# Optimization experiments

Measured on AMD Instinct MI355X. Metric: run time of the kernel, lower is better.

## Reference

```python
import jax, jax.numpy as jnp
import numpy as np

B, C, O, H, W, K, KS = 32, 128, 128, 56, 56, 4, 3
EPS = 1e-5


def setup_inputs() -> dict:
    key = jax.random.key(0)
    ks = jax.random.split(key, 6)
    sc = lambda k, shape, s: jax.random.normal(k, shape, jnp.float32) * s
    return {
        "x": jax.random.normal(ks[0], (B, C, H, W), jnp.float32),
        "fc1_w": sc(ks[1], (K, C), 0.05),
        "fc1_b": jnp.zeros((K,), jnp.float32),
        "fc2_w": sc(ks[2], (K, K), 0.3),
        "fc2_b": jnp.zeros((K,), jnp.float32),
        "weight": sc(ks[3], (K, O, C, KS, KS), 0.05),  # [K, out, in/groups, kh, kw]
        "bias": sc(ks[4], (K, O), 0.05),
        "gamma": jnp.ones((O,), jnp.float32),
        "beta": jnp.zeros((O,), jnp.float32),
    }


def reference(x, fc1_w, fc1_b, fc2_w, fc2_b, weight, bias, gamma, beta):
    # attention2d: global avg pool -> 1x1 conv (== linear) -> relu -> 1x1 conv -> softmax over K
    pooled = x.mean(axis=(2, 3))                          # [B, C]
    h = jax.nn.relu(pooled @ fc1_w.T + fc1_b)             # [B, K]
    attn = jax.nn.softmax(h @ fc2_w.T + fc2_b, axis=-1)   # [B, K]

    # per-sample aggregated kernel / bias
    agg_w = jnp.einsum('bk,koihw->boihw', attn, weight)   # [B, O, C, KS, KS]
    agg_b = attn @ bias                                    # [B, O]

    # per-sample conv (== groups=batch trick in torch)
    def conv_one(xi, wi):
        return jax.lax.conv_general_dilated(
            xi[None], wi, window_strides=(1, 1),
            padding=((1, 1), (1, 1)),
            dimension_numbers=('NCHW', 'OIHW', 'NCHW'))[0]

    out = jax.vmap(conv_one)(x, agg_w) + agg_b[:, :, None, None]  # [B, O, H, W]

    # BatchNorm2d in training mode: biased batch stats over (N, H, W)
    mean = out.mean(axis=(0, 2, 3))
    var = out.var(axis=(0, 2, 3))
    out = (out - mean[None, :, None, None]) * jax.lax.rsqrt(var + EPS)[None, :, None, None]
    out = out * gamma[None, :, None, None] + beta[None, :, None, None]
    return jax.nn.relu(out)
```

## Files before the change

kernel.cpp:

```cpp
#include <hip/hip_runtime.h>
#include <hip/hip_bf16.h>

#define BB 32
#define CC 128
#define OO 128
#define HH 56
#define WW 56
#define KK 4
#define HW 3136
#define WPLANE 147456
#define EPSV 1e-5f

#define NPOS 348
#define BUFB 22528

typedef __attribute__((ext_vector_type(8))) short short8v;
typedef __attribute__((ext_vector_type(4))) float f32x4;

static __device__ __forceinline__ void gload16(const void* g, void* l) {
    __builtin_amdgcn_global_load_lds((const __attribute__((address_space(1))) void*)g,
                                     (__attribute__((address_space(3))) void*)l, 16, 0, 0);
}

__global__ void convert_pool_kernel(const float* __restrict__ x,
                                    ushort* __restrict__ xbf,
                                    float* __restrict__ pooledp,
                                    ushort* __restrict__ zpage) {
    const int h = blockIdx.x, b = blockIdx.y;
    if (h == 0 && b == 0 && threadIdx.x < 32) zpage[threadIdx.x] = 0;
    __shared__ float xl[128 * 57];
    const float* xp = x + (size_t)(b * CC) * HW + h * WW;
    #pragma unroll
    for (int k = 0; k < 28; ++k) {
        int e = threadIdx.x + k * 256;
        int c = e / 56, w = e - c * 56;
        xl[c * 57 + w] = xp[(size_t)c * HW + w];
    }
    __syncthreads();
    ushort* op = xbf + ((size_t)(b * HH + h)) * WW * CC;
    #pragma unroll
    for (int k = 0; k < 7; ++k) {
        int f = threadIdx.x + k * 256;
        int w = f >> 5, c4 = (f & 31) * 4;
        ushort4 v;
        __hip_bfloat16 b0 = __float2bfloat16(xl[(c4 + 0) * 57 + w]);
        __hip_bfloat16 b1 = __float2bfloat16(xl[(c4 + 1) * 57 + w]);
        __hip_bfloat16 b2 = __float2bfloat16(xl[(c4 + 2) * 57 + w]);
        __hip_bfloat16 b3 = __float2bfloat16(xl[(c4 + 3) * 57 + w]);
        v.x = *(ushort*)&b0; v.y = *(ushort*)&b1;
        v.z = *(ushort*)&b2; v.w = *(ushort*)&b3;
        *(ushort4*)(op + (size_t)w * CC + c4) = v;
    }
    if (threadIdx.x < 128) {
        int c = threadIdx.x;
        float s = 0.f;
        #pragma unroll
        for (int w = 0; w < 56; ++w) s += xl[c * 57 + w];
        pooledp[((size_t)(b * HH + h)) * CC + c] = s;
    }
}

__global__ void attn_kernel(const float* __restrict__ pooledp,
                            const float* __restrict__ fc1_w, const float* __restrict__ fc1_b,
                            const float* __restrict__ fc2_w, const float* __restrict__ fc2_b,
                            float* __restrict__ attn) {
    const int b = blockIdx.x, c = threadIdx.x;
    float s = 0.f;
    for (int h = 0; h < HH; ++h) s += pooledp[((size_t)(b * HH + h)) * CC + c];
    const float pc = s * (1.0f / HW);
    __shared__ float red[8];
    const int lane = c & 63, wid = c >> 6;
    #pragma unroll
    for (int k = 0; k < KK; ++k) {
        float v = pc * fc1_w[k * CC + c];
        for (int off = 32; off > 0; off >>= 1) v += __shfl_down(v, off, 64);
        if (lane == 0) red[k * 2 + wid] = v;
    }
    __syncthreads();
    if (c == 0) {
        float hk[KK], z[KK], m = -1e30f, den = 0.f;
        #pragma unroll
        for (int k = 0; k < KK; ++k)
            hk[k] = fmaxf(red[k * 2] + red[k * 2 + 1] + fc1_b[k], 0.f);
        #pragma unroll
        for (int k = 0; k < KK; ++k) {
            float t = fc2_b[k];
            #pragma unroll
            for (int j = 0; j < KK; ++j) t += hk[j] * fc2_w[k * KK + j];
            z[k] = t; m = fmaxf(m, t);
        }
        #pragma unroll
        for (int k = 0; k < KK; ++k) { z[k] = expf(z[k] - m); den += z[k]; }
        #pragma unroll
        for (int k = 0; k < KK; ++k) attn[b * KK + k] = z[k] / den;
    }
}

__global__ void aggw_kernel(const float* __restrict__ attn, const float* __restrict__ weight,
                            const float* __restrict__ bias,
                            ushort* __restrict__ aggw, float* __restrict__ agg_b) {
    int idx = blockIdx.x * 256 + threadIdx.x;
    if (idx < BB * 9 * OO * CC) {
        int cc = idx & 31;
        int t1 = idx >> 5;
        int o  = t1 & 127;
        int t2 = t1 >> 7;
        int ci = t2 & 3;
        int t3 = t2 >> 2;
        int j  = t3 % 9;
        int b  = t3 / 9;
        int c  = ci * 32 + cc;
        size_t wi = ((size_t)(o * CC + c)) * 9 + j;
        float s = attn[b*KK + 0] * weight[wi]
                + attn[b*KK + 1] * weight[wi + (size_t)WPLANE]
                + attn[b*KK + 2] * weight[wi + (size_t)2*WPLANE]
                + attn[b*KK + 3] * weight[wi + (size_t)3*WPLANE];
        __hip_bfloat16 hb = __float2bfloat16(s);
        aggw[idx] = *(ushort*)&hb;
    }
    if (blockIdx.x < 16) {
        int i = blockIdx.x * 256 + threadIdx.x;
        int b = i >> 7, o = i & 127;
        float s = 0.f;
        #pragma unroll
        for (int k = 0; k < KK; ++k) s += attn[b*KK + k] * bias[k*OO + o];
        agg_b[i] = s;
    }
}

__launch_bounds__(256, 2)
__global__ void conv_kernel(const ushort* __restrict__ xbf, const ushort* __restrict__ aggw,
                            const float* __restrict__ agg_b, const ushort* __restrict__ zpage,
                            float* __restrict__ out,
                            float* __restrict__ psum, float* __restrict__ psumsq) {
    const int lid  = blockIdx.x;
    const int gwid = (lid & 7) * 56 + (lid >> 3);
    const int b = gwid / 14;
    const int t = gwid - b * 14;
    const int h0 = t * 4;
    __shared__ ushort xs[2 * BUFB / 2];

    const int tid  = threadIdx.x;
    const int lane = tid & 63;
    const int wid  = tid >> 6;
    const int wg = wid & 1;
    const int wy = wid >> 1;
    const int cf = lane & 15;
    const int kg = lane >> 4;

    const ushort* gp[6]; int gstep[6];
    #pragma unroll
    for (int k = 0; k < 6; ++k) {
        int q = wid + 4 * k;
        int un = q * 64 + lane;
        int u = un ^ ((un >> 3) & 7);
        int pos = u >> 2, quad = u & 3;
        int row = pos / 58, col = pos - row * 58;
        int gh = h0 - 1 + row, gw = col - 1;
        bool valid = (pos < NPOS) && (gh >= 0) && (gh < HH) && (gw >= 0) && (gw < WW);
        gp[k] = valid ? (xbf + ((size_t)((b * HH + gh) * WW + gw)) * CC + quad * 8) : zpage;
        gstep[k] = valid ? 32 : 0;
    }

    int blin[7];
    #pragma unroll
    for (int nf = 0; nf < 7; ++nf) {
        int p = wy * 112 + nf * 16 + cf;
        int r = p / 56, w = p - r * 56;
        blin[nf] = (((r + 1) * 58 + (w + 1)) << 6) + kg * 16;
    }

    f32x4 acc[4][7];
    #pragma unroll
    for (int mf = 0; mf < 4; ++mf)
        #pragma unroll
        for (int nf = 0; nf < 7; ++nf) acc[mf][nf] = (f32x4){0.f, 0.f, 0.f, 0.f};

    const ushort* Ab = aggw + ((size_t)b * 36) * 4096 + (size_t)(wg * 64 + cf) * 32 + kg * 8;
    #define ALOAD(mf_, j_, ci_) (*(const short8v*)(Ab + (size_t)((j_) * 4 + (ci_)) * 4096 + (mf_) * 512))

    short8v pa[4];
    #pragma unroll
    for (int mf = 0; mf < 4; ++mf) pa[mf] = ALOAD(mf, 0, 0);

    #pragma unroll
    for (int k = 0; k < 6; ++k) {
        int q = wid + 4 * k;
        if (q < 22) { gload16(gp[k], (char*)xs + q * 1024); gp[k] += gstep[k]; }
    }
    __syncthreads();

    int cur = 0;
    for (int ci = 0; ci < 4; ++ci) {
        if (ci < 3) {
            char* base = (char*)xs + (cur ^ 1) * BUFB;
            #pragma unroll
            for (int k = 0; k < 6; ++k) {
                int q = wid + 4 * k;
                if (q < 22) { gload16(gp[k], base + q * 1024); gp[k] += gstep[k]; }
            }
        }
        const char* xbuf = (const char*)xs + cur * BUFB;

        short8v bfc[7], bfn[7];
        #pragma unroll
        for (int nf = 0; nf < 7; ++nf) {
            int lin = blin[nf] + (-58 - 1) * 64;
            int swz = lin ^ ((lin >> 3) & 0x70);
            bfc[nf] = *(const short8v*)(xbuf + swz);
        }
        #pragma unroll
        for (int j = 0; j < 9; ++j) {
            if (j < 8) {
                const int toff = (((j+1)/3 - 1) * 58 + ((j+1)%3 - 1)) * 64;
                #pragma unroll
                for (int nf = 0; nf < 7; ++nf) {
                    int lin = blin[nf] + toff;
                    int swz = lin ^ ((lin >> 3) & 0x70);
                    bfn[nf] = *(const short8v*)(xbuf + swz);
                }
            }
            short8v ca[4];
            #pragma unroll
            for (int mf = 0; mf < 4; ++mf) ca[mf] = pa[mf];
            if (j < 8) {
                #pragma unroll
                for (int mf = 0; mf < 4; ++mf) pa[mf] = ALOAD(mf, j + 1, ci);
            } else if (ci < 3) {
                #pragma unroll
                for (int mf = 0; mf < 4; ++mf) pa[mf] = ALOAD(mf, 0, ci + 1);
            }
            #pragma unroll
            for (int nf = 0; nf < 7; ++nf) {
                #pragma unroll
                for (int mf = 0; mf < 4; ++mf)
                    acc[mf][nf] = __builtin_amdgcn_mfma_f32_16x16x32_bf16(ca[mf], bfc[nf], acc[mf][nf], 0, 0, 0);
            }
            if (j < 8) {
                #pragma unroll
                for (int nf = 0; nf < 7; ++nf) bfc[nf] = bfn[nf];
            }
        }
        if (ci < 3) __syncthreads();
        cur ^= 1;
    }

    #pragma unroll
    for (int mf = 0; mf < 4; ++mf) {
        #pragma unroll
        for (int i = 0; i < 4; ++i) {
            const int o = wg * 64 + mf * 16 + kg * 4 + i;
            const float ab = agg_b[b * OO + o];
            float* op = out + ((size_t)(b * OO + o)) * HW;
            float s = 0.f, s2 = 0.f;
            #pragma unroll
            for (int nf = 0; nf < 7; ++nf) {
                int p = wy * 112 + nf * 16 + cf;
                int r = p / 56, w = p - r * 56;
                float v = acc[mf][nf][i] + ab;
                op[(h0 + r) * WW + w] = v;
                s += v; s2 += v * v;
            }
            s  += __shfl_xor(s, 1, 64);  s  += __shfl_xor(s, 2, 64);
            s  += __shfl_xor(s, 4, 64);  s  += __shfl_xor(s, 8, 64);
            s2 += __shfl_xor(s2, 1, 64); s2 += __shfl_xor(s2, 2, 64);
            s2 += __shfl_xor(s2, 4, 64); s2 += __shfl_xor(s2, 8, 64);
            if (cf == 0) {
                int row = (b * 14 + t) * 2 + wy;
                psum[row * OO + o]   = s;
                psumsq[row * OO + o] = s2;
            }
        }
    }
}

__global__ void finstats_kernel(const float* __restrict__ psum, const float* __restrict__ psumsq,
                                float* __restrict__ sums, float* __restrict__ sumsq) {
    const int o = blockIdx.x, l = threadIdx.x;
    float s = 0.f, s2 = 0.f;
    for (int r = l; r < 896; r += 64) { s += psum[r * OO + o]; s2 += psumsq[r * OO + o]; }
    for (int off = 32; off > 0; off >>= 1) {
        s  += __shfl_down(s, off, 64);
        s2 += __shfl_down(s2, off, 64);
    }
    if (l == 0) { sums[o] = s; sumsq[o] = s2; }
}

__global__ void bn_kernel(float* __restrict__ out,
                          const float* __restrict__ sums, const float* __restrict__ sumsq,
                          const float* __restrict__ gamma, const float* __restrict__ beta) {
    const float invN = 1.0f / (float)(BB * HW);
    const int total4 = BB * OO * HW / 4;
    for (int i = blockIdx.x * blockDim.x + threadIdx.x; i < total4; i += gridDim.x * blockDim.x) {
        int o = (i / (HW/4)) % OO;
        float mean = sums[o] * invN;
        float var  = sumsq[o] * invN - mean*mean;
        float inv  = rsqrtf(var + EPSV);
        float g  = gamma[o] * inv;
        float bt = beta[o] - mean * g;
        float4 v = ((float4*)out)[i];
        v.x = fmaxf(v.x*g + bt, 0.f);
        v.y = fmaxf(v.y*g + bt, 0.f);
        v.z = fmaxf(v.z*g + bt, 0.f);
        v.w = fmaxf(v.w*g + bt, 0.f);
        ((float4*)out)[i] = v;
    }
}

extern "C" void kernel_launch(void* const* d_in, const int* in_sizes, int n_in,
                              void* d_out, int out_size, void* d_ws, size_t ws_size,
                              hipStream_t stream) {
    const float* x      = (const float*)d_in[0];
    const float* fc1_w  = (const float*)d_in[1];
    const float* fc1_b  = (const float*)d_in[2];
    const float* fc2_w  = (const float*)d_in[3];
    const float* fc2_b  = (const float*)d_in[4];
    const float* weight = (const float*)d_in[5];
    const float* bias   = (const float*)d_in[6];
    const float* gamma  = (const float*)d_in[7];
    const float* beta   = (const float*)d_in[8];
    float* out = (float*)d_out;

    const size_t XBF_ELEMS  = (size_t)BB * HW * CC;
    const size_t AGGW_ELEMS = (size_t)BB * 9 * OO * CC;
    ushort* xbf  = (ushort*)d_ws;
    ushort* aggw = xbf + XBF_ELEMS;
    float*  wsf  = (float*)(aggw + AGGW_ELEMS);
    float* pooledp = wsf;
    float* attn    = pooledp + 229376;
    float* agg_b   = attn + 128;
    float* psum    = agg_b + 4096;
    float* psumsq  = psum + 114688;
    float* sums    = psumsq + 114688;
    float* sumsq   = sums + 128;
    ushort* zpage  = (ushort*)(sumsq + 128);

    convert_pool_kernel<<<dim3(HH, BB), 256, 0, stream>>>(x, xbf, pooledp, zpage);
    attn_kernel<<<BB, 128, 0, stream>>>(pooledp, fc1_w, fc1_b, fc2_w, fc2_b, attn);
    aggw_kernel<<<(int)((AGGW_ELEMS + 255)/256), 256, 0, stream>>>(attn, weight, bias, aggw, agg_b);
    conv_kernel<<<dim3(448), 256, 0, stream>>>(xbf, aggw, agg_b, zpage, out, psum, psumsq);
    finstats_kernel<<<OO, 64, 0, stream>>>(psum, psumsq, sums, sumsq);
    bn_kernel<<<2048, 256, 0, stream>>>(out, sums, sumsq, gamma, beta);
}
```

Measured before the change: 111.2 us.

## Fuse conv, batch-stat reduction and BN/ReLU into one cooperative kernel

Replaces the conv, finstats and bn launches with a single cooperative-launch kernel. It keeps conv accumulators in registers, reduces per-channel stats across the grid with two grid syncs, then writes normalized ReLU output directly. This removes the round trip of writing and rereading the full fp32 output. To fit co-residency it switches the fused path to a single LDS buffer without double-buffered prefetch, and it falls back to the old three kernels if the cooperative launch fails. The convert/pool kernel also now uses float4 loads into a swizzled LDS layout and writes 16-byte bf16 vectors.

```diff
diff --git a/kernel.cpp b/kernel.cpp
--- a/kernel.cpp
+++ b/kernel.cpp
@@ -1,5 +1,8 @@
 #include <hip/hip_runtime.h>
 #include <hip/hip_bf16.h>
+#include <hip/hip_cooperative_groups.h>
+
+namespace cg = cooperative_groups;
 
 #define BB 32
 #define CC 128
@@ -28,34 +31,45 @@
                                     ushort* __restrict__ zpage) {
     const int h = blockIdx.x, b = blockIdx.y;
     if (h == 0 && b == 0 && threadIdx.x < 32) zpage[threadIdx.x] = 0;
-    __shared__ float xl[128 * 57];
+    __shared__ float4 xl4[1792];
     const float* xp = x + (size_t)(b * CC) * HW + h * WW;
-    #pragma unroll
-    for (int k = 0; k < 28; ++k) {
-        int e = threadIdx.x + k * 256;
-        int c = e / 56, w = e - c * 56;
-        xl[c * 57 + w] = xp[(size_t)c * HW + w];
+
+    #pragma unroll
+    for (int k = 0; k < 7; ++k) {
+        int u = threadIdx.x + k * 256;
+        int c = u / 14, w4 = u - c * 14;
+        float4 v = *(const float4*)(xp + (size_t)c * HW + w4 * 4);
+        xl4[u ^ ((c >> 3) & 7)] = v;
     }
     __syncthreads();
-    ushort* op = xbf + ((size_t)(b * HH + h)) * WW * CC;
-    #pragma unroll
-    for (int k = 0; k < 7; ++k) {
-        int f = threadIdx.x + k * 256;
-        int w = f >> 5, c4 = (f & 31) * 4;
-        ushort4 v;
-        __hip_bfloat16 b0 = __float2bfloat16(xl[(c4 + 0) * 57 + w]);
-        __hip_bfloat16 b1 = __float2bfloat16(xl[(c4 + 1) * 57 + w]);
-        __hip_bfloat16 b2 = __float2bfloat16(xl[(c4 + 2) * 57 + w]);
-        __hip_bfloat16 b3 = __float2bfloat16(xl[(c4 + 3) * 57 + w]);
-        v.x = *(ushort*)&b0; v.y = *(ushort*)&b1;
-        v.z = *(ushort*)&b2; v.w = *(ushort*)&b3;
-        *(ushort4*)(op + (size_t)w * CC + c4) = v;
-    }
+
+    const float* xf = (const float*)xl4;
+    #pragma unroll
+    for (int k = 0; k < 4; ++k) {
+        int v = threadIdx.x + k * 256;
+        if (v < 896) {
+            int w = v >> 4, c8 = v & 15;
+            int w4 = w >> 2, wo = w & 3;
+            short8v res;
+            #pragma unroll
+            for (int j = 0; j < 8; ++j) {
+                int c = c8 * 8 + j;
+                int su = (c * 14 + w4) ^ (c8 & 7);
+                __hip_bfloat16 hb = __float2bfloat16(xf[su * 4 + wo]);
+                res[j] = *(short*)&hb;
+            }
+            *(short8v*)(xbf + ((size_t)((b * HH + h) * WW + w)) * CC + c8 * 8) = res;
+        }
+    }
+
     if (threadIdx.x < 128) {
         int c = threadIdx.x;
         float s = 0.f;
         #pragma unroll
-        for (int w = 0; w < 56; ++w) s += xl[c * 57 + w];
+        for (int w4 = 0; w4 < 14; ++w4) {
+            float4 v = xl4[(c * 14 + w4) ^ ((c >> 3) & 7)];
+            s += v.x + v.y + v.z + v.w;
+        }
         pooledp[((size_t)(b * HH + h)) * CC + c] = s;
     }
 }
@@ -128,6 +142,115 @@
     }
 }
 
+template <bool DBUF>
+static __device__ __forceinline__ void conv_body(
+        const ushort* __restrict__ xbf, const ushort* __restrict__ aggw,
+        const ushort* __restrict__ zpage, ushort* xs,
+        int b, int h0, int wg, int wy, int cf, int kg, int wid, int lane,
+        f32x4 (&acc)[4][7]) {
+    const ushort* gp[6]; int gstep[6];
+    #pragma unroll
+    for (int k = 0; k < 6; ++k) {
+        int q = wid + 4 * k;
+        int un = q * 64 + lane;
+        int u = un ^ ((un >> 3) & 7);
+        int pos = u >> 2, quad = u & 3;
+        int row = pos / 58, col = pos - row * 58;
+        int gh = h0 - 1 + row, gw = col - 1;
+        bool valid = (pos < NPOS) && (gh >= 0) && (gh < HH) && (gw >= 0) && (gw < WW);
+        gp[k] = valid ? (xbf + ((size_t)((b * HH + gh) * WW + gw)) * CC + quad * 8) : zpage;
+        gstep[k] = valid ? 32 : 0;
+    }
+
+    int blin[7];
+    #pragma unroll
+    for (int nf = 0; nf < 7; ++nf) {
+        int p = wy * 112 + nf * 16 + cf;
+        int r = p / 56, w = p - r * 56;
+        blin[nf] = (((r + 1) * 58 + (w + 1)) << 6) + kg * 16;
+    }
+
+    const ushort* Ab = aggw + ((size_t)b * 36) * 4096 + (size_t)(wg * 64 + cf) * 32 + kg * 8;
+    #define ALOAD(mf_, j_, ci_) (*(const short8v*)(Ab + (size_t)((j_) * 4 + (ci_)) * 4096 + (mf_) * 512))
+
+    short8v pa[4];
+    #pragma unroll
+    for (int mf = 0; mf < 4; ++mf) pa[mf] = ALOAD(mf, 0, 0);
+
+    #pragma unroll
+    for (int k = 0; k < 6; ++k) {
+        int q = wid + 4 * k;
+        if (q < 22) { gload16(gp[k], (char*)xs + q * 1024); gp[k] += gstep[k]; }
+    }
+    __syncthreads();
+
+    int cur = 0;
+    for (int ci = 0; ci < 4; ++ci) {
+        if (DBUF && ci < 3) {
+            char* base = (char*)xs + (cur ^ 1) * BUFB;
+            #pragma unroll
+            for (int k = 0; k < 6; ++k) {
+                int q = wid + 4 * k;
+                if (q < 22) { gload16(gp[k], base + q * 1024); gp[k] += gstep[k]; }
+            }
+        }
+        const char* xbuf = (const char*)xs + (DBUF ? cur * BUFB : 0);
+
+        short8v bfc[7], bfn[7];
+        #pragma unroll
+        for (int nf = 0; nf < 7; ++nf) {
+            int lin = blin[nf] + (-58 - 1) * 64;
+            int swz = lin ^ ((lin >> 3) & 0x70);
+            bfc[nf] = *(const short8v*)(xbuf + swz);
+        }
+        #pragma unroll
+        for (int j = 0; j < 9; ++j) {
+            if (j < 8) {
+                const int toff = (((j+1)/3 - 1) * 58 + ((j+1)%3 - 1)) * 64;
+                #pragma unroll
+                for (int nf = 0; nf < 7; ++nf) {
+                    int lin = blin[nf] + toff;
+                    int swz = lin ^ ((lin >> 3) & 0x70);
+                    bfn[nf] = *(const short8v*)(xbuf + swz);
+                }
+            }
+            short8v ca[4];
+            #pragma unroll
+            for (int mf = 0; mf < 4; ++mf) ca[mf] = pa[mf];
+            if (j < 8) {
+                #pragma unroll
+                for (int mf = 0; mf < 4; ++mf) pa[mf] = ALOAD(mf, j + 1, ci);
+            } else if (ci < 3) {
+                #pragma unroll
+                for (int mf = 0; mf < 4; ++mf) pa[mf] = ALOAD(mf, 0, ci + 1);
+            }
+            #pragma unroll
+            for (int nf = 0; nf < 7; ++nf) {
+                #pragma unroll
+                for (int mf = 0; mf < 4; ++mf)
+                    acc[mf][nf] = __builtin_amdgcn_mfma_f32_16x16x32_bf16(ca[mf], bfc[nf], acc[mf][nf], 0, 0, 0);
+            }
+            if (j < 8) {
+                #pragma unroll
+                for (int nf = 0; nf < 7; ++nf) bfc[nf] = bfn[nf];
+            }
+        }
+        if (ci < 3) {
+            if (!DBUF) {
+                __syncthreads();
+                #pragma unroll
+                for (int k = 0; k < 6; ++k) {
+                    int q = wid + 4 * k;
+                    if (q < 22) { gload16(gp[k], (char*)xs + q * 1024); gp[k] += gstep[k]; }
+                }
+            }
+            __syncthreads();
+            cur ^= 1;
+        }
+    }
+    #undef ALOAD
+}
+
 __launch_bounds__(256, 2)
 __global__ void conv_kernel(const ushort* __restrict__ xbf, const ushort* __restrict__ aggw,
                             const float* __restrict__ agg_b, const ushort* __restrict__ zpage,
@@ -143,32 +266,8 @@
     const int tid  = threadIdx.x;
     const int lane = tid & 63;
     const int wid  = tid >> 6;
-    const int wg = wid & 1;
-    const int wy = wid >> 1;
-    const int cf = lane & 15;
-    const int kg = lane >> 4;
-
-    const ushort* gp[6]; int gstep[6];
-    #pragma unroll
-    for (int k = 0; k < 6; ++k) {
-        int q = wid + 4 * k;
-        int un = q * 64 + lane;
-        int u = un ^ ((un >> 3) & 7);
-        int pos = u >> 2, quad = u & 3;
-        int row = pos / 58, col = pos - row * 58;
-        int gh = h0 - 1 + row, gw = col - 1;
-        bool valid = (pos < NPOS) && (gh >= 0) && (gh < HH) && (gw >= 0) && (gw < WW);
-        gp[k] = valid ? (xbf + ((size_t)((b * HH + gh) * WW + gw)) * CC + quad * 8) : zpage;
-        gstep[k] = valid ? 32 : 0;
-    }
-
-    int blin[7];
-    #pragma unroll
-    for (int nf = 0; nf < 7; ++nf) {
-        int p = wy * 112 + nf * 16 + cf;
-        int r = p / 56, w = p - r * 56;
-        blin[nf] = (((r + 1) * 58 + (w + 1)) << 6) + kg * 16;
-    }
+    const int wg = wid & 1, wy = wid >> 1;
+    const int cf = lane & 15, kg = lane >> 4;
 
     f32x4 acc[4][7];
     #pragma unroll
@@ -176,74 +275,7 @@
         #pragma unroll
         for (int nf = 0; nf < 7; ++nf) acc[mf][nf] = (f32x4){0.f, 0.f, 0.f, 0.f};
 
-    const ushort* Ab = aggw + ((size_t)b * 36) * 4096 + (size_t)(wg * 64 + cf) * 32 + kg * 8;
-    #define ALOAD(mf_, j_, ci_) (*(const short8v*)(Ab + (size_t)((j_) * 4 + (ci_)) * 4096 + (mf_) * 512))
-
-    short8v pa[4];
-    #pragma unroll
-    for (int mf = 0; mf < 4; ++mf) pa[mf] = ALOAD(mf, 0, 0);
-
-    #pragma unroll
-    for (int k = 0; k < 6; ++k) {
-        int q = wid + 4 * k;
-        if (q < 22) { gload16(gp[k], (char*)xs + q * 1024); gp[k] += gstep[k]; }
-    }
-    __syncthreads();
-
-    int cur = 0;
-    for (int ci = 0; ci < 4; ++ci) {
-        if (ci < 3) {
-            char* base = (char*)xs + (cur ^ 1) * BUFB;
-            #pragma unroll
-            for (int k = 0; k < 6; ++k) {
-                int q = wid + 4 * k;
-                if (q < 22) { gload16(gp[k], base + q * 1024); gp[k] += gstep[k]; }
-            }
-        }
-        const char* xbuf = (const char*)xs + cur * BUFB;
-
-        short8v bfc[7], bfn[7];
-        #pragma unroll
-        for (int nf = 0; nf < 7; ++nf) {
-            int lin = blin[nf] + (-58 - 1) * 64;
-            int swz = lin ^ ((lin >> 3) & 0x70);
-            bfc[nf] = *(const short8v*)(xbuf + swz);
-        }
-        #pragma unroll
-        for (int j = 0; j < 9; ++j) {
-            if (j < 8) {
-                const int toff = (((j+1)/3 - 1) * 58 + ((j+1)%3 - 1)) * 64;
-                #pragma unroll
-                for (int nf = 0; nf < 7; ++nf) {
-                    int lin = blin[nf] + toff;
-                    int swz = lin ^ ((lin >> 3) & 0x70);
-                    bfn[nf] = *(const short8v*)(xbuf + swz);
-                }
-            }
-            short8v ca[4];
-            #pragma unroll
-            for (int mf = 0; mf < 4; ++mf) ca[mf] = pa[mf];
-            if (j < 8) {
-                #pragma unroll
-                for (int mf = 0; mf < 4; ++mf) pa[mf] = ALOAD(mf, j + 1, ci);
-            } else if (ci < 3) {
-                #pragma unroll
-                for (int mf = 0; mf < 4; ++mf) pa[mf] = ALOAD(mf, 0, ci + 1);
-            }
-            #pragma unroll
-            for (int nf = 0; nf < 7; ++nf) {
-                #pragma unroll
-                for (int mf = 0; mf < 4; ++mf)
-                    acc[mf][nf] = __builtin_amdgcn_mfma_f32_16x16x32_bf16(ca[mf], bfc[nf], acc[mf][nf], 0, 0, 0);
-            }
-            if (j < 8) {
-                #pragma unroll
-                for (int nf = 0; nf < 7; ++nf) bfc[nf] = bfn[nf];
-            }
-        }
-        if (ci < 3) __syncthreads();
-        cur ^= 1;
-    }
+    conv_body<true>(xbf, aggw, zpage, xs, b, h0, wg, wy, cf, kg, wid, lane, acc);
 
     #pragma unroll
     for (int mf = 0; mf < 4; ++mf) {
@@ -269,6 +301,109 @@
                 int row = (b * 14 + t) * 2 + wy;
                 psum[row * OO + o]   = s;
                 psumsq[row * OO + o] = s2;
+            }
+        }
+    }
+}
+
+__launch_bounds__(256, 2)
+__global__ void conv_bn_kernel(const ushort* __restrict__ xbf, const ushort* __restrict__ aggw,
+                               const float* __restrict__ agg_b, const ushort* __restrict__ zpage,
+                               float* __restrict__ out,
+                               float* __restrict__ psum, float* __restrict__ psumsq,
+                               float* __restrict__ sums, float* __restrict__ sumsq,
+                               const float* __restrict__ gamma, const float* __restrict__ beta) {
+    const int lid  = blockIdx.x;
+    const int gwid = (lid & 7) * 56 + (lid >> 3);
+    const int b = gwid / 14;
+    const int t = gwid - b * 14;
+    const int h0 = t * 4;
+    __shared__ ushort xs[BUFB / 2];
+
+    const int tid  = threadIdx.x;
+    const int lane = tid & 63;
+    const int wid  = tid >> 6;
+    const int wg = wid & 1, wy = wid >> 1;
+    const int cf = lane & 15, kg = lane >> 4;
+
+    f32x4 acc[4][7];
+    #pragma unroll
+    for (int mf = 0; mf < 4; ++mf)
+        #pragma unroll
+        for (int nf = 0; nf < 7; ++nf) acc[mf][nf] = (f32x4){0.f, 0.f, 0.f, 0.f};
+
+    conv_body<false>(xbf, aggw, zpage, xs, b, h0, wg, wy, cf, kg, wid, lane, acc);
+
+    #pragma unroll
+    for (int mf = 0; mf < 4; ++mf) {
+        #pragma unroll
+        for (int i = 0; i < 4; ++i) {
+            const int o = wg * 64 + mf * 16 + kg * 4 + i;
+            const float ab = agg_b[b * OO + o];
+            float s = 0.f, s2 = 0.f;
+            #pragma unroll
+            for (int nf = 0; nf < 7; ++nf) {
+                float v = acc[mf][nf][i] + ab;
+                acc[mf][nf][i] = v;
+                s += v; s2 += v * v;
+            }
+            s  += __shfl_xor(s, 1, 64);  s  += __shfl_xor(s, 2, 64);
+            s  += __shfl_xor(s, 4, 64);  s  += __shfl_xor(s, 8, 64);
+            s2 += __shfl_xor(s2, 1, 64); s2 += __shfl_xor(s2, 2, 64);
+            s2 += __shfl_xor(s2, 4, 64); s2 += __shfl_xor(s2, 8, 64);
+            if (cf == 0) {
+                int row = (b * 14 + t) * 2 + wy;
+                psum[row * OO + o]   = s;
+                psumsq[row * OO + o] = s2;
+            }
+        }
+    }
+
+    cg::grid_group grid = cg::this_grid();
+    grid.sync();
+
+    if (lid < 128) {
+        const int o = lid;
+        float s = 0.f, s2 = 0.f;
+        for (int r = tid; r < 896; r += 256) {
+            s  += psum[r * OO + o];
+            s2 += psumsq[r * OO + o];
+        }
+        for (int off = 32; off > 0; off >>= 1) {
+            s  += __shfl_down(s, off, 64);
+            s2 += __shfl_down(s2, off, 64);
+        }
+        float* red = (float*)xs;
+        if (lane == 0) { red[wid] = s; red[8 + wid] = s2; }
+        __syncthreads();
+        if (tid == 0) {
+            sums[o]  = red[0] + red[1] + red[2] + red[3];
+            sumsq[o] = red[8] + red[9] + red[10] + red[11];
+        }
+    }
+    grid.sync();
+
+    float* sl = (float*)xs;
+    if (tid < 128) { sl[tid] = sums[tid]; sl[128 + tid] = sumsq[tid]; }
+    __syncthreads();
+
+    const float invN = 1.0f / (float)(BB * HW);
+    #pragma unroll
+    for (int mf = 0; mf < 4; ++mf) {
+        #pragma unroll
+        for (int i = 0; i < 4; ++i) {
+            const int o = wg * 64 + mf * 16 + kg * 4 + i;
+            float mean = sl[o] * invN;
+            float var  = sl[128 + o] * invN - mean * mean;
+            float inv  = rsqrtf(var + EPSV);
+            float g  = gamma[o] * inv;
+            float bt = beta[o] - mean * g;
+            float* op = out + ((size_t)(b * OO + o)) * HW;
+            #pragma unroll
+            for (int nf = 0; nf < 7; ++nf) {
+                int p = wy * 112 + nf * 16 + cf;
+                int r = p / 56, w = p - r * 56;
+                op[(h0 + r) * WW + w] = fmaxf(acc[mf][nf][i] * g + bt, 0.f);
             }
         }
     }
@@ -338,7 +473,16 @@
     convert_pool_kernel<<<dim3(HH, BB), 256, 0, stream>>>(x, xbf, pooledp, zpage);
     attn_kernel<<<BB, 128, 0, stream>>>(pooledp, fc1_w, fc1_b, fc2_w, fc2_b, attn);
     aggw_kernel<<<(int)((AGGW_ELEMS + 255)/256), 256, 0, stream>>>(attn, weight, bias, aggw, agg_b);
-    conv_kernel<<<dim3(448), 256, 0, stream>>>(xbf, aggw, agg_b, zpage, out, psum, psumsq);
-    finstats_kernel<<<OO, 64, 0, stream>>>(psum, psumsq, sums, sumsq);
-    bn_kernel<<<2048, 256, 0, stream>>>(out, sums, sumsq, gamma, beta);
-}
+
+    void* cargs[] = { (void*)&xbf, (void*)&aggw, (void*)&agg_b, (void*)&zpage,
+                      (void*)&out, (void*)&psum, (void*)&psumsq,
+                      (void*)&sums, (void*)&sumsq, (void*)&gamma, (void*)&beta };
+    hipError_t cerr = hipLaunchCooperativeKernel((const void*)conv_bn_kernel,
+                                                 dim3(448), dim3(256), cargs, 0, stream);
+    if (cerr != hipSuccess) {
+        (void)hipGetLastError();
+        conv_kernel<<<dim3(448), 256, 0, stream>>>(xbf, aggw, agg_b, zpage, out, psum, psumsq);
+        finstats_kernel<<<OO, 64, 0, stream>>>(psum, psumsq, sums, sumsq);
+        bn_kernel<<<2048, 256, 0, stream>>>(out, sums, sumsq, gamma, beta);
+    }
+}
```

Measured after the change: 247.5 us. 2.22x slower.

## Stage conv output in bf16 workspace and vectorize input conversion with swizzled LDS

Applied to the files above, without the earlier changes.

The conv kernel can now write its pre-BN output as bf16 into a workspace buffer, and a new BN kernel reads the bf16 values and writes the final fp32 output. The aim is to cut the intermediate write and read traffic roughly in half. This path runs only when the workspace is large enough; otherwise the old fp32 path is used. Separately, the convert/pool kernel now uses float4 global loads into an XOR-swizzled LDS tile and packs eight bf16 values per 16-byte store. The trade-off is bf16 rounding of the pre-normalization values, while the BN statistics are still computed in fp32.

```diff
diff --git a/kernel.cpp b/kernel.cpp
--- a/kernel.cpp
+++ b/kernel.cpp
@@ -28,34 +28,45 @@
                                     ushort* __restrict__ zpage) {
     const int h = blockIdx.x, b = blockIdx.y;
     if (h == 0 && b == 0 && threadIdx.x < 32) zpage[threadIdx.x] = 0;
-    __shared__ float xl[128 * 57];
+    __shared__ float4 xl4[1792];
     const float* xp = x + (size_t)(b * CC) * HW + h * WW;
-    #pragma unroll
-    for (int k = 0; k < 28; ++k) {
-        int e = threadIdx.x + k * 256;
-        int c = e / 56, w = e - c * 56;
-        xl[c * 57 + w] = xp[(size_t)c * HW + w];
+
+    #pragma unroll
+    for (int k = 0; k < 7; ++k) {
+        int u = threadIdx.x + k * 256;
+        int c = u / 14, w4 = u - c * 14;
+        float4 v = *(const float4*)(xp + (size_t)c * HW + w4 * 4);
+        xl4[u ^ ((c >> 3) & 7)] = v;
     }
     __syncthreads();
-    ushort* op = xbf + ((size_t)(b * HH + h)) * WW * CC;
-    #pragma unroll
-    for (int k = 0; k < 7; ++k) {
-        int f = threadIdx.x + k * 256;
-        int w = f >> 5, c4 = (f & 31) * 4;
-        ushort4 v;
-        __hip_bfloat16 b0 = __float2bfloat16(xl[(c4 + 0) * 57 + w]);
-        __hip_bfloat16 b1 = __float2bfloat16(xl[(c4 + 1) * 57 + w]);
-        __hip_bfloat16 b2 = __float2bfloat16(xl[(c4 + 2) * 57 + w]);
-        __hip_bfloat16 b3 = __float2bfloat16(xl[(c4 + 3) * 57 + w]);
-        v.x = *(ushort*)&b0; v.y = *(ushort*)&b1;
-        v.z = *(ushort*)&b2; v.w = *(ushort*)&b3;
-        *(ushort4*)(op + (size_t)w * CC + c4) = v;
-    }
+
+    const float* xf = (const float*)xl4;
+    #pragma unroll
+    for (int k = 0; k < 4; ++k) {
+        int v = threadIdx.x + k * 256;
+        if (v < 896) {
+            int w = v >> 4, c8 = v & 15;
+            int w4 = w >> 2, wo = w & 3;
+            short8v res;
+            #pragma unroll
+            for (int j = 0; j < 8; ++j) {
+                int c = c8 * 8 + j;
+                int su = (c * 14 + w4) ^ (c8 & 7);
+                __hip_bfloat16 hb = __float2bfloat16(xf[su * 4 + wo]);
+                res[j] = *(short*)&hb;
+            }
+            *(short8v*)(xbf + ((size_t)((b * HH + h) * WW + w)) * CC + c8 * 8) = res;
+        }
+    }
+
     if (threadIdx.x < 128) {
         int c = threadIdx.x;
         float s = 0.f;
         #pragma unroll
-        for (int w = 0; w < 56; ++w) s += xl[c * 57 + w];
+        for (int w4 = 0; w4 < 14; ++w4) {
+            float4 v = xl4[(c * 14 + w4) ^ ((c >> 3) & 7)];
+            s += v.x + v.y + v.z + v.w;
+        }
         pooledp[((size_t)(b * HH + h)) * CC + c] = s;
     }
 }
@@ -128,26 +139,11 @@
     }
 }
 
-__launch_bounds__(256, 2)
-__global__ void conv_kernel(const ushort* __restrict__ xbf, const ushort* __restrict__ aggw,
-                            const float* __restrict__ agg_b, const ushort* __restrict__ zpage,
-                            float* __restrict__ out,
-                            float* __restrict__ psum, float* __restrict__ psumsq) {
-    const int lid  = blockIdx.x;
-    const int gwid = (lid & 7) * 56 + (lid >> 3);
-    const int b = gwid / 14;
-    const int t = gwid - b * 14;
-    const int h0 = t * 4;
-    __shared__ ushort xs[2 * BUFB / 2];
-
-    const int tid  = threadIdx.x;
-    const int lane = tid & 63;
-    const int wid  = tid >> 6;
-    const int wg = wid & 1;
-    const int wy = wid >> 1;
-    const int cf = lane & 15;
-    const int kg = lane >> 4;
-
+static __device__ __forceinline__ void conv_body(
+        const ushort* __restrict__ xbf, const ushort* __restrict__ aggw,
+        const ushort* __restrict__ zpage, ushort* xs,
+        int b, int h0, int wg, int wy, int cf, int kg, int wid, int lane,
+        f32x4 (&acc)[4][7]) {
     const ushort* gp[6]; int gstep[6];
     #pragma unroll
     for (int k = 0; k < 6; ++k) {
@@ -170,12 +166,6 @@
         blin[nf] = (((r + 1) * 58 + (w + 1)) << 6) + kg * 16;
     }
 
-    f32x4 acc[4][7];
-    #pragma unroll
-    for (int mf = 0; mf < 4; ++mf)
-        #pragma unroll
-        for (int nf = 0; nf < 7; ++nf) acc[mf][nf] = (f32x4){0.f, 0.f, 0.f, 0.f};
-
     const ushort* Ab = aggw + ((size_t)b * 36) * 4096 + (size_t)(wg * 64 + cf) * 32 + kg * 8;
     #define ALOAD(mf_, j_, ci_) (*(const short8v*)(Ab + (size_t)((j_) * 4 + (ci_)) * 4096 + (mf_) * 512))
 
@@ -244,6 +234,35 @@
         if (ci < 3) __syncthreads();
         cur ^= 1;
     }
+    #undef ALOAD
+}
+
+template <bool BF16OUT>
+__launch_bounds__(256, 2)
+__global__ void conv_kernel(const ushort* __restrict__ xbf, const ushort* __restrict__ aggw,
+                            const float* __restrict__ agg_b, const ushort* __restrict__ zpage,
+                            void* __restrict__ outv,
+                            float* __restrict__ psum, float* __restrict__ psumsq) {
+    const int lid  = blockIdx.x;
+    const int gwid = (lid & 7) * 56 + (lid >> 3);
+    const int b = gwid / 14;
+    const int t = gwid - b * 14;
+    const int h0 = t * 4;
+    __shared__ ushort xs[2 * BUFB / 2];
+
+    const int tid  = threadIdx.x;
+    const int lane = tid & 63;
+    const int wid  = tid >> 6;
+    const int wg = wid & 1, wy = wid >> 1;
+    const int cf = lane & 15, kg = lane >> 4;
+
+    f32x4 acc[4][7];
+    #pragma unroll
+    for (int mf = 0; mf < 4; ++mf)
+        #pragma unroll
+        for (int nf = 0; nf < 7; ++nf) acc[mf][nf] = (f32x4){0.f, 0.f, 0.f, 0.f};
+
+    conv_body(xbf, aggw, zpage, xs, b, h0, wg, wy, cf, kg, wid, lane, acc);
 
     #pragma unroll
     for (int mf = 0; mf < 4; ++mf) {
@@ -251,14 +270,19 @@
         for (int i = 0; i < 4; ++i) {
             const int o = wg * 64 + mf * 16 + kg * 4 + i;
             const float ab = agg_b[b * OO + o];
-            float* op = out + ((size_t)(b * OO + o)) * HW;
+            const size_t obase = ((size_t)(b * OO + o)) * HW;
             float s = 0.f, s2 = 0.f;
             #pragma unroll
             for (int nf = 0; nf < 7; ++nf) {
                 int p = wy * 112 + nf * 16 + cf;
                 int r = p / 56, w = p - r * 56;
                 float v = acc[mf][nf][i] + ab;
-                op[(h0 + r) * WW + w] = v;
+                if (BF16OUT) {
+                    __hip_bfloat16 hb = __float2bfloat16(v);
+                    ((ushort*)outv)[obase + (h0 + r) * WW + w] = *(ushort*)&hb;
+                } else {
+                    ((float*)outv)[obase + (h0 + r) * WW + w] = v;
+                }
                 s += v; s2 += v * v;
             }
             s  += __shfl_xor(s, 1, 64);  s  += __shfl_xor(s, 2, 64);
@@ -284,6 +308,37 @@
         s2 += __shfl_down(s2, off, 64);
     }
     if (l == 0) { sums[o] = s; sumsq[o] = s2; }
+}
+
+__global__ void bn_bf16_kernel(const ushort* __restrict__ convout, float* __restrict__ out,
+                               const float* __restrict__ sums, const float* __restrict__ sumsq,
+                               const float* __restrict__ gamma, const float* __restrict__ beta) {
+    const float invN = 1.0f / (float)(BB * HW);
+    const int total8 = BB * OO * HW / 8;
+    for (int i = blockIdx.x * blockDim.x + threadIdx.x; i < total8; i += gridDim.x * blockDim.x) {
+        int o = (i / (HW/8)) % OO;
+        float mean = sums[o] * invN;
+        float var  = sumsq[o] * invN - mean*mean;
+        float inv  = rsqrtf(var + EPSV);
+        float g  = gamma[o] * inv;
+        float bt = beta[o] - mean * g;
+        short8v v = *(const short8v*)(convout + (size_t)i * 8);
+        float4 lo, hi;
+        #pragma unroll
+        for (int j = 0; j < 4; ++j) {
+            ushort u = (ushort)v[j];
+            float f = __bfloat162float(*(__hip_bfloat16*)&u);
+            ((float*)&lo)[j] = fmaxf(f * g + bt, 0.f);
+        }
+        #pragma unroll
+        for (int j = 0; j < 4; ++j) {
+            ushort u = (ushort)v[4 + j];
+            float f = __bfloat162float(*(__hip_bfloat16*)&u);
+            ((float*)&hi)[j] = fmaxf(f * g + bt, 0.f);
+        }
+        ((float4*)out)[i * 2]     = lo;
+        ((float4*)out)[i * 2 + 1] = hi;
+    }
 }
 
 __global__ void bn_kernel(float* __restrict__ out,
@@ -323,6 +378,7 @@
 
     const size_t XBF_ELEMS  = (size_t)BB * HW * CC;
     const size_t AGGW_ELEMS = (size_t)BB * 9 * OO * CC;
+    const size_t OUT_ELEMS  = (size_t)BB * OO * HW;
     ushort* xbf  = (ushort*)d_ws;
     ushort* aggw = xbf + XBF_ELEMS;
     float*  wsf  = (float*)(aggw + AGGW_ELEMS);
@@ -334,11 +390,24 @@
     float* sums    = psumsq + 114688;
     float* sumsq   = sums + 128;
     ushort* zpage  = (ushort*)(sumsq + 128);
+    ushort* convout = (ushort*)(zpage + 32);
+
+    const size_t need = (size_t)((char*)(convout + OUT_ELEMS) - (char*)d_ws);
+    const bool bf16path = ws_size >= need;
 
     convert_pool_kernel<<<dim3(HH, BB), 256, 0, stream>>>(x, xbf, pooledp, zpage);
     attn_kernel<<<BB, 128, 0, stream>>>(pooledp, fc1_w, fc1_b, fc2_w, fc2_b, attn);
     aggw_kernel<<<(int)((AGGW_ELEMS + 255)/256), 256, 0, stream>>>(attn, weight, bias, aggw, agg_b);
-    conv_kernel<<<dim3(448), 256, 0, stream>>>(xbf, aggw, agg_b, zpage, out, psum, psumsq);
-    finstats_kernel<<<OO, 64, 0, stream>>>(psum, psumsq, sums, sumsq);
-    bn_kernel<<<2048, 256, 0, stream>>>(out, sums, sumsq, gamma, beta);
-}
+
+    if (bf16path) {
+        conv_kernel<true><<<dim3(448), 256, 0, stream>>>(xbf, aggw, agg_b, zpage,
+                                                         (void*)convout, psum, psumsq);
+        finstats_kernel<<<OO, 64, 0, stream>>>(psum, psumsq, sums, sumsq);
+        bn_bf16_kernel<<<2048, 256, 0, stream>>>(convout, out, sums, sumsq, gamma, beta);
+    } else {
+        conv_kernel<false><<<dim3(448), 256, 0, stream>>>(xbf, aggw, agg_b, zpage,
+                                                          (void*)out, psum, psumsq);
+        finstats_kernel<<<OO, 64, 0, stream>>>(psum, psumsq, sums, sumsq);
+        bn_kernel<<<2048, 256, 0, stream>>>(out, sums, sumsq, gamma, beta);
+    }
+}
```

After: 99.77 us. 10.3% less time.
